# Kernel tuning notes

Hardware: AMD Instinct MI355X
Metric: run time of the kernel (lower is better)

Reference implementation:

```python
import jax, jax.numpy as jnp
import numpy as np

B, D, H, E, K = 8192, 1024, 256, 16, 4


def setup_inputs() -> dict:
    key = jax.random.key(0)
    ks = jax.random.split(key, 6)
    s_d = D ** -0.5
    s_h = H ** -0.5
    return {
        "x": jax.random.normal(ks[0], (B, D), dtype=jnp.float32),
        "route_w": jax.random.normal(ks[1], (E, D), dtype=jnp.float32) * s_d,
        "w1": jax.random.normal(ks[2], (E, H, D), dtype=jnp.float32) * s_d,
        "b1": jax.random.normal(ks[3], (E, H), dtype=jnp.float32) * s_d,
        "w2": jax.random.normal(ks[4], (E, D, H), dtype=jnp.float32) * s_h,
        "b2": jax.random.normal(ks[5], (E, D), dtype=jnp.float32) * s_h,
    }


def _moe_forward(x, route_w, w1, b1, w2, b2):
    # Router: logits (B, E) -> top-k softmax weights scattered back to (B, E).
    logits = x @ route_w.T
    top_vals, top_idx = jax.lax.top_k(logits, K)
    top_w = jax.nn.softmax(top_vals, axis=-1)
    rows = jnp.arange(x.shape[0])[:, None]
    weights = jnp.zeros_like(logits).at[rows, top_idx].set(top_w)  # (B, E)

    # Experts: out = sum_e w[:, e] * relu(relu(x W1e^T + b1e) W2e^T + b2e)
    # Non-selected experts have weight 0, so dense-then-weight matches the
    # original masked gather/scatter math exactly (dropout = 0).
    def step(out, params_e):
        W1, bb1, W2, bb2, we = params_e
        h = jax.nn.relu(x @ W1.T + bb1)       # (B, H)
        y = jax.nn.relu(h @ W2.T + bb2)       # (B, D)
        return out + y * we[:, None], None

    out0 = jnp.zeros_like(x)
    out, _ = jax.lax.scan(step, out0, (w1, b1, w2, b2, weights.T))
    return out


def reference(x, route_w, w1, b1, w2, b2):
    return _moe_forward(x, route_w, w1, b1, w2, b2)
```

## Files before the change

kernel.cpp:

```cpp
#include <hip/hip_runtime.h>
#include <stdint.h>

typedef unsigned short u16;
typedef __attribute__((ext_vector_type(8))) short bf16x8;
typedef __attribute__((ext_vector_type(4))) float f32x4;
typedef __attribute__((ext_vector_type(8))) u16 u16x8;
typedef __attribute__((ext_vector_type(4))) u16 u16x4;

#define NTOK 8192
#define DDIM 1024
#define HDIM 256
#define NEXP 16
#define MAXT 272
#define MAXSLOT (MAXT * 128)

__device__ __forceinline__ u16 f2bf(float f) {
  uint32_t u = __builtin_bit_cast(uint32_t, f);
  u += 0x7FFFu + ((u >> 16) & 1u);
  return (u16)(u >> 16);
}
__device__ __forceinline__ float bf2f(u16 h) {
  return __builtin_bit_cast(float, (uint32_t)h << 16);
}

__device__ __forceinline__ void gll16(const void* g, void* l) {
  __builtin_amdgcn_global_load_lds((const __attribute__((address_space(1))) void*)g,
                                   (__attribute__((address_space(3))) void*)l,
                                   16, 0, 0);
}

__global__ __launch_bounds__(256) void cvt_kernel(const float* __restrict__ in,
                                                  u16* __restrict__ out) {
  size_t i = ((size_t)blockIdx.x * 256 + threadIdx.x) * 8;
  const float4 a = *(const float4*)(in + i);
  const float4 b = *(const float4*)(in + i + 4);
  u16x8 o;
  o[0] = f2bf(a.x); o[1] = f2bf(a.y); o[2] = f2bf(a.z); o[3] = f2bf(a.w);
  o[4] = f2bf(b.x); o[5] = f2bf(b.y); o[6] = f2bf(b.z); o[7] = f2bf(b.w);
  *(u16x8*)(out + i) = o;
}

__global__ __launch_bounds__(256) void zero_out_kernel(float* __restrict__ p) {
  size_t i = ((size_t)blockIdx.x * 256 + threadIdx.x) * 4;
  *(float4*)(p + i) = (float4){0.f, 0.f, 0.f, 0.f};
}

__global__ __launch_bounds__(256) void router_kernel(const float* __restrict__ x,
                                                     const float* __restrict__ rw,
                                                     int* __restrict__ epack,
                                                     float* __restrict__ ew,
                                                     u16* __restrict__ xbf) {
  __shared__ __align__(16) uint8_t rwlds[65536];
  const int tid = threadIdx.x;

#pragma unroll
  for (int i = 0; i < 16; ++i) {
    int byte = (i * 256 + tid) * 16;
    int sw = byte ^ (((byte >> 8) & 7) << 4);
    *(float4*)(rwlds + sw) = *(const float4*)((const uint8_t*)rw + byte);
  }
  __syncthreads();

  const int lane = tid & 63, wid = tid >> 6;
  const int s = lane & 15;
  const int tok = blockIdx.x * 16 + wid * 4 + (lane >> 4);
  const float* xrow = x + (size_t)tok * DDIM;
  u16* xbrow = xbf + (size_t)tok * DDIM;

  double acc[NEXP];
#pragma unroll
  for (int e = 0; e < NEXP; ++e) acc[e] = 0.0;

#pragma unroll 4
  for (int g = 0; g < 16; ++g) {
    const int d = s * 64 + g * 4;
    float4 xv = *(const float4*)(xrow + d);
    u16x4 o;
    o[0] = f2bf(xv.x); o[1] = f2bf(xv.y); o[2] = f2bf(xv.z); o[3] = f2bf(xv.w);
    *(u16x4*)(xbrow + d) = o;
    const double x0 = xv.x, x1 = xv.y, x2 = xv.z, x3 = xv.w;
    const int roff = (s * 256 + g * 16) ^ ((s & 7) << 4);
#pragma unroll
    for (int e = 0; e < NEXP; ++e) {
      float4 rv = *(const float4*)(rwlds + e * 4096 + roff);
      acc[e] = fma(x0, (double)rv.x, acc[e]);
      acc[e] = fma(x1, (double)rv.y, acc[e]);
      acc[e] = fma(x2, (double)rv.z, acc[e]);
      acc[e] = fma(x3, (double)rv.w, acc[e]);
    }
  }

#define FOLD(H, M)                                                   \
  _Pragma("unroll") for (int i = 0; i < H; ++i) {                    \
    double send = (lane & M) ? acc[i] : acc[i + H];                  \
    double recv = __shfl_xor(send, M);                               \
    acc[i] = ((lane & M) ? acc[i + H] : acc[i]) + recv;              \
  }
  FOLD(8, 1)
  FOLD(4, 2)
  FOLD(2, 4)
  FOLD(1, 8)
#undef FOLD
  const int e_mine = ((lane & 1) << 3) | ((lane & 2) << 1) |
                     ((lane & 4) >> 1) | ((lane & 8) >> 3);

  double val = acc[0];
  double tv[4]; int tidx[4];
#pragma unroll
  for (int k = 0; k < 4; ++k) {
    double bv = val; int be = e_mine;
#pragma unroll
    for (int m = 1; m < 16; m <<= 1) {
      double ov = __shfl_xor(bv, m);
      int oe = __shfl_xor(be, m);
      if (ov > bv || (ov == bv && oe < be)) { bv = ov; be = oe; }
    }
    tv[k] = bv; tidx[k] = be;
    if (e_mine == be) val = -1.0e300;
  }

  if ((lane & 15) == 0) {
    float m0 = (float)tv[0];
    float w[4]; float sum = 0.f;
#pragma unroll
    for (int k = 0; k < 4; ++k) { w[k] = expf((float)tv[k] - m0); sum += w[k]; }
    epack[tok] = tidx[0] | (tidx[1] << 8) | (tidx[2] << 16) | (tidx[3] << 24);
#pragma unroll
    for (int k = 0; k < 4; ++k) ew[tok * 4 + k] = w[k] / sum;
  }
}

__global__ __launch_bounds__(1024) void compact_kernel(const int* __restrict__ epack,
                                                       const float* __restrict__ ew,
                                                       int* __restrict__ texp,
                                                       int* __restrict__ perm,
                                                       float* __restrict__ wsl,
                                                       int* __restrict__ islot) {
  __shared__ int wave_cnt[16][NEXP];
  __shared__ int counts_sm[NEXP];
  __shared__ int wtot[16], wave_off[16];
  const int e = blockIdx.x;
  const int tid = threadIdx.x, lane = tid & 63, w = tid >> 6;

  int ep[8]; unsigned m[8];
#pragma unroll
  for (int j = 0; j < 8; ++j) {
    ep[j] = epack[tid * 8 + j];
    m[j] = (1u << (ep[j] & 255)) | (1u << ((ep[j] >> 8) & 255)) |
           (1u << ((ep[j] >> 16) & 255)) | (1u << ((ep[j] >> 24) & 255));
  }
#pragma unroll
  for (int ee = 0; ee < NEXP; ++ee) {
    int c = 0;
#pragma unroll
    for (int j = 0; j < 8; ++j) c += (m[j] >> ee) & 1u;
#pragma unroll
    for (int off = 32; off > 0; off >>= 1) c += __shfl_xor(c, off);
    if (lane == 0) wave_cnt[w][ee] = c;
  }
  unsigned fm = 0;
#pragma unroll
  for (int j = 0; j < 8; ++j) fm |= ((m[j] >> e) & 1u) << j;
  int s = __popc(fm);
  int incl = s;
#pragma unroll
  for (int d = 1; d < 64; d <<= 1) {
    int t2 = __shfl_up(incl, d);
    if (lane >= d) incl += t2;
  }
  if (lane == 63) wtot[w] = incl;
  __syncthreads();
  if (tid < NEXP) {
    int c = 0;
    for (int w2 = 0; w2 < 16; ++w2) c += wave_cnt[w2][tid];
    counts_sm[tid] = c;
  }
  if (tid == 0) {
    int run = 0;
    for (int w2 = 0; w2 < 16; ++w2) { wave_off[w2] = run; run += wtot[w2]; }
  }
  __syncthreads();
  int base = 0;
  for (int ee = 0; ee < NEXP; ++ee)
    if (ee < e) base += ((counts_sm[ee] + 127) >> 7) << 7;
  int pos = base + wave_off[w] + (incl - s);
#pragma unroll
  for (int j = 0; j < 8; ++j) {
    if ((fm >> j) & 1u) {
      int tok = tid * 8 + j;
      int b0 = ep[j] & 255, b1 = (ep[j] >> 8) & 255, b2_ = (ep[j] >> 16) & 255;
      int k = (b0 == e) ? 0 : ((b1 == e) ? 1 : ((b2_ == e) ? 2 : 3));
      perm[pos] = tok;
      wsl[pos] = ew[tok * 4 + k];
      islot[tok * 4 + k] = pos;
      ++pos;
    }
  }
  int cnt = counts_sm[e];
  int pad = (((cnt + 127) >> 7) << 7) - cnt;
  if (tid < pad) { perm[base + cnt + tid] = 0; wsl[base + cnt + tid] = 0.f; }
  if (e == 0 && tid == 0) {
    int tc = 0;
    for (int ee = 0; ee < NEXP; ++ee) {
      int nt = (counts_sm[ee] + 127) >> 7;
      for (int i = 0; i < nt; ++i) texp[tc++] = ee;
    }
    for (; tc < MAXT; ++tc) texp[tc] = -1;
  }
}

__device__ __forceinline__ void stage_rows(const u16* __restrict__ base, int ld,
                                           int kbase, uint8_t* dst, int tid) {
#pragma unroll
  for (int i = 0; i < 4; ++i) {
    int u = i * 256 + tid;
    int row = u >> 3, g = u & 7;
    gll16(base + (size_t)row * ld + kbase + ((g ^ (row & 7)) << 3), dst + u * 16);
  }
}
__device__ __forceinline__ void stage_gather(const u16* __restrict__ xbf,
                                             const int tok[4], int kbase,
                                             uint8_t* dst, int tid) {
#pragma unroll
  for (int i = 0; i < 4; ++i) {
    int u = i * 256 + tid;
    int row = u >> 3, g = u & 7;
    gll16(xbf + (size_t)tok[i] * DDIM + kbase + ((g ^ (row & 7)) << 3), dst + u * 16);
  }
}

__device__ __forceinline__ void mma_tile(const uint8_t* Ab, const uint8_t* Bb,
                                         f32x4 acc[4][4], int wm, int wn,
                                         int lrow, int lk) {
#pragma unroll
  for (int s = 0; s < 2; ++s) {
    bf16x8 af[4], bfr[4];
#pragma unroll
    for (int f = 0; f < 4; ++f) {
      int ar = wm * 64 + f * 16 + lrow;
      af[f] = *(const bf16x8*)(Ab + ar * 128 + ((((s << 2) | lk) ^ (ar & 7)) << 4));
      int br = wn * 64 + f * 16 + lrow;
      bfr[f] = *(const bf16x8*)(Bb + br * 128 + ((((s << 2) | lk) ^ (br & 7)) << 4));
    }
#pragma unroll
    for (int i = 0; i < 4; ++i)
#pragma unroll
      for (int j = 0; j < 4; ++j)
        acc[i][j] = __builtin_amdgcn_mfma_f32_16x16x32_bf16(af[i], bfr[j], acc[i][j], 0, 0, 0);
  }
}

__global__ __launch_bounds__(256) void gemm1_kernel(const u16* __restrict__ xbf,
                                                    const u16* __restrict__ w1bf,
                                                    const float* __restrict__ b1,
                                                    const int* __restrict__ texp,
                                                    const int* __restrict__ perm,
                                                    u16* __restrict__ Hc, int t0) {
  __shared__ __align__(16) uint8_t smem[2][32768];
  const int t = t0 + blockIdx.x;
  const int e = (t < MAXT) ? texp[t] : -1;
  if (e < 0) return;
  const int n0 = blockIdx.y * 128;
  const int tid = threadIdx.x;
  const int lane = tid & 63, wid = tid >> 6;
  const int wm = wid >> 1, wn = wid & 1;
  const int lrow = lane & 15, lk = lane >> 4;

  int tok[4];
#pragma unroll
  for (int i = 0; i < 4; ++i) tok[i] = perm[t * 128 + ((i * 256 + tid) >> 3)];
  const u16* Bsrc = w1bf + ((size_t)e * HDIM + n0) * DDIM;

  f32x4 acc[4][4];
#pragma unroll
  for (int i = 0; i < 4; ++i)
#pragma unroll
    for (int j = 0; j < 4; ++j) acc[i][j] = (f32x4){0.f, 0.f, 0.f, 0.f};

  stage_gather(xbf, tok, 0, smem[0], tid);
  stage_rows(Bsrc, DDIM, 0, smem[0] + 16384, tid);
  __syncthreads();
  int cur = 0;
  for (int kt = 0; kt < 16; ++kt) {
    if (kt < 15) {
      stage_gather(xbf, tok, (kt + 1) * 64, smem[cur ^ 1], tid);
      stage_rows(Bsrc, DDIM, (kt + 1) * 64, smem[cur ^ 1] + 16384, tid);
    }
    mma_tile(smem[cur], smem[cur] + 16384, acc, wm, wn, lrow, lk);
    __syncthreads();
    cur ^= 1;
  }
#pragma unroll
  for (int j = 0; j < 4; ++j) {
    int n = n0 + wn * 64 + j * 16 + lrow;
    float bias = b1[e * HDIM + n];
#pragma unroll
    for (int i = 0; i < 4; ++i) {
      int rloc = blockIdx.x * 128 + wm * 64 + i * 16 + lk * 4;
#pragma unroll
      for (int r = 0; r < 4; ++r) {
        float h = fmaxf(acc[i][j][r] + bias, 0.f);
        Hc[((size_t)rloc + r) * HDIM + n] = f2bf(h);
      }
    }
  }
}

template <int MODE>
__global__ __launch_bounds__(256) void gemm2_kernel(const u16* __restrict__ Hc,
                                                    const u16* __restrict__ w2bf,
                                                    const float* __restrict__ b2,
                                                    const int* __restrict__ texp,
                                                    const int* __restrict__ perm,
                                                    const float* __restrict__ wsl,
                                                    float* __restrict__ out,
                                                    u16* __restrict__ ybuf,
                                                    int t0, int n0, int NC) {
  __shared__ __align__(16) uint8_t smem[2][32768];
  const int t = t0 + blockIdx.x;
  const int e = (t < MAXT) ? texp[t] : -1;
  if (e < 0) return;
  const int tid = threadIdx.x;
  const int lane = tid & 63, wid = tid >> 6;
  const int wm = wid >> 1, wn = wid & 1;
  const int lrow = lane & 15, lk = lane >> 4;

  const u16* Asrc = Hc + (size_t)blockIdx.x * 128 * HDIM;
  const u16* Bsrc = w2bf + ((size_t)e * DDIM + n0 + blockIdx.y * 128) * HDIM;

  f32x4 acc[4][4];
#pragma unroll
  for (int i = 0; i < 4; ++i)
#pragma unroll
    for (int j = 0; j < 4; ++j) acc[i][j] = (f32x4){0.f, 0.f, 0.f, 0.f};

  stage_rows(Asrc, HDIM, 0, smem[0], tid);
  stage_rows(Bsrc, HDIM, 0, smem[0] + 16384, tid);
  __syncthreads();
  int cur = 0;
  for (int kt = 0; kt < 4; ++kt) {
    if (kt < 3) {
      stage_rows(Asrc, HDIM, (kt + 1) * 64, smem[cur ^ 1], tid);
      stage_rows(Bsrc, HDIM, (kt + 1) * 64, smem[cur ^ 1] + 16384, tid);
    }
    mma_tile(smem[cur], smem[cur] + 16384, acc, wm, wn, lrow, lk);
    __syncthreads();
    cur ^= 1;
  }
  float bias[4];
#pragma unroll
  for (int j = 0; j < 4; ++j)
    bias[j] = b2[e * DDIM + n0 + blockIdx.y * 128 + wn * 64 + j * 16 + lrow];
#pragma unroll
  for (int i = 0; i < 4; ++i) {
#pragma unroll
    for (int r = 0; r < 4; ++r) {
      int slot = t * 128 + wm * 64 + i * 16 + lk * 4 + r;
      if (MODE == 0) {
        int tokn = perm[slot];
        float w = wsl[slot];
#pragma unroll
        for (int j = 0; j < 4; ++j) {
          int n = n0 + blockIdx.y * 128 + wn * 64 + j * 16 + lrow;
          float h = fmaxf(acc[i][j][r] + bias[j], 0.f);
          atomicAdd(&out[(size_t)tokn * DDIM + n], w * h);
        }
      } else {
#pragma unroll
        for (int j = 0; j < 4; ++j) {
          int nloc = blockIdx.y * 128 + wn * 64 + j * 16 + lrow;
          float h = fmaxf(acc[i][j][r] + bias[j], 0.f);
          ybuf[(size_t)slot * NC + nloc] = f2bf(h);
        }
      }
    }
  }
}

__global__ __launch_bounds__(256) void combine_kernel(const u16* __restrict__ ybuf,
                                                      const float* __restrict__ ew,
                                                      const int* __restrict__ islot,
                                                      float* __restrict__ out,
                                                      int n0, int NC, int cshift) {
  int gid = blockIdx.x * 256 + threadIdx.x;
  int t = gid >> cshift;
  int c = (gid & ((1 << cshift) - 1)) << 2;
  const int4 sl = *(const int4*)(islot + t * 4);
  const float4 w = *(const float4*)(ew + t * 4);
  float4 a = {0.f, 0.f, 0.f, 0.f};
#define ACC(SL, W)                                             \
  {                                                            \
    u16x4 y = *(const u16x4*)(ybuf + (size_t)(SL)*NC + c);     \
    a.x += (W)*bf2f(y[0]); a.y += (W)*bf2f(y[1]);              \
    a.z += (W)*bf2f(y[2]); a.w += (W)*bf2f(y[3]);              \
  }
  ACC(sl.x, w.x); ACC(sl.y, w.y); ACC(sl.z, w.z); ACC(sl.w, w.w);
#undef ACC
  *(float4*)(out + (size_t)t * DDIM + n0 + c) = a;
}

extern "C" void kernel_launch(void* const* d_in, const int* in_sizes, int n_in,
                              void* d_out, int out_size, void* d_ws, size_t ws_size,
                              hipStream_t stream) {
  const float* x = (const float*)d_in[0];
  const float* route_w = (const float*)d_in[1];
  const float* w1 = (const float*)d_in[2];
  const float* b1 = (const float*)d_in[3];
  const float* w2 = (const float*)d_in[4];
  const float* b2 = (const float*)d_in[5];
  float* out = (float*)d_out;

  uint8_t* ws = (uint8_t*)d_ws;
  const size_t OFF_EPACK = 0;
  const size_t OFF_EW    = 32768;
  const size_t OFF_ISLOT = 163840;
  const size_t OFF_TEXP  = 294912;
  const size_t OFF_PERM  = 296960;
  const size_t OFF_WSL   = 436224;
  const size_t OFF_X     = 1048576;
  const size_t OFF_W1    = OFF_X + (size_t)NTOK * DDIM * 2;
  const size_t OFF_W2    = OFF_W1 + (size_t)NEXP * HDIM * DDIM * 2;
  const size_t OFF_HC    = OFF_W2 + (size_t)NEXP * DDIM * HDIM * 2;
  const size_t OFF_Y     = OFF_HC + (size_t)MAXSLOT * HDIM * 2;

  int* epack  = (int*)(ws + OFF_EPACK);
  float* ew   = (float*)(ws + OFF_EW);
  int* islot  = (int*)(ws + OFF_ISLOT);
  int* texp   = (int*)(ws + OFF_TEXP);
  int* perm   = (int*)(ws + OFF_PERM);
  float* wsl  = (float*)(ws + OFF_WSL);
  u16* xbf    = (u16*)(ws + OFF_X);
  u16* w1bf   = (u16*)(ws + OFF_W1);
  u16* w2bf   = (u16*)(ws + OFF_W2);
  u16* Hc     = (u16*)(ws + OFF_HC);
  u16* ybuf   = (u16*)(ws + OFF_Y);

  cvt_kernel<<<dim3((NEXP * HDIM * DDIM) / 2048), 256, 0, stream>>>(w1, w1bf);
  cvt_kernel<<<dim3((NEXP * DDIM * HDIM) / 2048), 256, 0, stream>>>(w2, w2bf);
  router_kernel<<<dim3(NTOK / 16), 256, 0, stream>>>(x, route_w, epack, ew, xbf);
  compact_kernel<<<dim3(NEXP), 1024, 0, stream>>>(epack, ew, texp, perm, wsl, islot);

  int NC = 0;
  for (int cand = 1024; cand >= 128; cand >>= 1) {
    if (ws_size >= OFF_Y + (size_t)MAXSLOT * cand * 2) { NC = cand; break; }
  }

  if (NC > 0) {
    gemm1_kernel<<<dim3(MAXT, HDIM / 128), 256, 0, stream>>>(xbf, w1bf, b1, texp, perm, Hc, 0);
    int cshift = __builtin_ctz(NC >> 2);
    for (int n0 = 0; n0 < DDIM; n0 += NC) {
      gemm2_kernel<1><<<dim3(MAXT, NC / 128), 256, 0, stream>>>(
          Hc, w2bf, b2, texp, perm, wsl, out, ybuf, 0, n0, NC);
      combine_kernel<<<dim3((NTOK << cshift) / 256), 256, 0, stream>>>(
          ybuf, ew, islot, out, n0, NC, cshift);
    }
  } else {
    long room = (long)ws_size - (long)OFF_HC;
    int CT = (int)(room / 65536);
    if (CT > MAXT) CT = MAXT;
    if (CT < 16) CT = 16;
    zero_out_kernel<<<dim3((NTOK * DDIM) / 1024), 256, 0, stream>>>(out);
    for (int t0 = 0; t0 < MAXT; t0 += CT) {
      int ct = (MAXT - t0 < CT) ? (MAXT - t0) : CT;
      gemm1_kernel<<<dim3(ct, HDIM / 128), 256, 0, stream>>>(xbf, w1bf, b1, texp, perm, Hc, t0);
      gemm2_kernel<0><<<dim3(ct, DDIM / 128), 256, 0, stream>>>(
          Hc, w2bf, b2, texp, perm, wsl, out, ybuf, t0, 0, DDIM);
    }
  }
}
```

Before: 145.3 us.

## Keep H tile resident in LDS and sweep all output columns per block in GEMM2

Replaces the 2D-grid GEMM2 with a 512-thread kernel that loads the block's full 128x256 H tile into shared memory once, then streams W2 column chunks through a double buffer, writing each 128-column output chunk after its four k-steps. This removes the repeated reload of the H tile across column blocks and caps the ybuf chunk width at 512, so the combine pass runs in at least two rounds. In exchange it uses 96KB of LDS per block and launches only one block per token tile, which lowers parallelism and occupancy.

```diff
diff --git a/kernel.cpp b/kernel.cpp
--- a/kernel.cpp
+++ b/kernel.cpp
@@ -218,6 +218,15 @@
     gll16(base + (size_t)row * ld + kbase + ((g ^ (row & 7)) << 3), dst + u * 16);
   }
 }
+__device__ __forceinline__ void stage_rows512(const u16* __restrict__ base, int ld,
+                                              int kbase, uint8_t* dst, int tid) {
+#pragma unroll
+  for (int i = 0; i < 2; ++i) {
+    int u = i * 512 + tid;
+    int row = u >> 3, g = u & 7;
+    gll16(base + (size_t)row * ld + kbase + ((g ^ (row & 7)) << 3), dst + u * 16);
+  }
+}
 __device__ __forceinline__ void stage_gather(const u16* __restrict__ xbf,
                                              const int tok[4], int kbase,
                                              uint8_t* dst, int tid) {
@@ -244,6 +253,30 @@
     }
 #pragma unroll
     for (int i = 0; i < 4; ++i)
+#pragma unroll
+      for (int j = 0; j < 4; ++j)
+        acc[i][j] = __builtin_amdgcn_mfma_f32_16x16x32_bf16(af[i], bfr[j], acc[i][j], 0, 0, 0);
+  }
+}
+
+__device__ __forceinline__ void mma_step8(const uint8_t* Ab, const uint8_t* Bb,
+                                          f32x4 acc[2][4], int wm, int wn,
+                                          int lrow, int lk) {
+#pragma unroll
+  for (int s = 0; s < 2; ++s) {
+    bf16x8 af[2], bfr[4];
+#pragma unroll
+    for (int f = 0; f < 2; ++f) {
+      int ar = wm * 32 + f * 16 + lrow;
+      af[f] = *(const bf16x8*)(Ab + ar * 128 + ((((s << 2) | lk) ^ (ar & 7)) << 4));
+    }
+#pragma unroll
+    for (int f = 0; f < 4; ++f) {
+      int br = wn * 64 + f * 16 + lrow;
+      bfr[f] = *(const bf16x8*)(Bb + br * 128 + ((((s << 2) | lk) ^ (br & 7)) << 4));
+    }
+#pragma unroll
+    for (int i = 0; i < 2; ++i)
 #pragma unroll
       for (int j = 0; j < 4; ++j)
         acc[i][j] = __builtin_amdgcn_mfma_f32_16x16x32_bf16(af[i], bfr[j], acc[i][j], 0, 0, 0);
@@ -306,16 +339,75 @@
   }
 }
 
-template <int MODE>
-__global__ __launch_bounds__(256) void gemm2_kernel(const u16* __restrict__ Hc,
-                                                    const u16* __restrict__ w2bf,
-                                                    const float* __restrict__ b2,
-                                                    const int* __restrict__ texp,
-                                                    const int* __restrict__ perm,
-                                                    const float* __restrict__ wsl,
-                                                    float* __restrict__ out,
-                                                    u16* __restrict__ ybuf,
-                                                    int t0, int n0, int NC) {
+__global__ __launch_bounds__(512) void gemm2_wide_kernel(const u16* __restrict__ Hc,
+                                                         const u16* __restrict__ w2bf,
+                                                         const float* __restrict__ b2,
+                                                         const int* __restrict__ texp,
+                                                         u16* __restrict__ ybuf,
+                                                         int nbase, int ncols) {
+  __shared__ __align__(16) uint8_t smem[98304];
+  const int t = blockIdx.x;
+  const int e = texp[t];
+  if (e < 0) return;
+  const int tid = threadIdx.x;
+  const int lane = tid & 63, wid = tid >> 6;
+  const int wm = wid >> 1, wn = wid & 1;
+  const int lrow = lane & 15, lk = lane >> 4;
+
+  const u16* Asrc = Hc + (size_t)t * 128 * HDIM;
+#pragma unroll
+  for (int c = 0; c < 4; ++c)
+    stage_rows512(Asrc, HDIM, c * 64, smem + c * 16384, tid);
+
+  const u16* W2base = w2bf + ((size_t)e * DDIM + nbase) * HDIM;
+  const int S = ncols >> 5;
+  stage_rows512(W2base, HDIM, 0, smem + 65536, tid);
+  __syncthreads();
+
+  f32x4 acc[2][4];
+#pragma unroll
+  for (int i = 0; i < 2; ++i)
+#pragma unroll
+    for (int j = 0; j < 4; ++j) acc[i][j] = (f32x4){0.f, 0.f, 0.f, 0.f};
+
+  int cur = 0;
+  for (int s = 0; s < S; ++s) {
+    const int kt = s & 3, nc = s >> 2;
+    if (s + 1 < S) {
+      const int kt2 = (s + 1) & 3, nc2 = (s + 1) >> 2;
+      stage_rows512(W2base + (size_t)(nc2 * 128) * HDIM, HDIM, kt2 * 64,
+                    smem + 65536 + ((cur ^ 1) << 14), tid);
+    }
+    mma_step8(smem + (kt << 14), smem + 65536 + (cur << 14), acc, wm, wn, lrow, lk);
+    if (kt == 3) {
+#pragma unroll
+      for (int j = 0; j < 4; ++j) {
+        const int nl = nc * 128 + wn * 64 + j * 16 + lrow;
+        const float bias = b2[e * DDIM + nbase + nl];
+#pragma unroll
+        for (int i = 0; i < 2; ++i) {
+          const int slotb = t * 128 + wm * 32 + i * 16 + lk * 4;
+#pragma unroll
+          for (int r = 0; r < 4; ++r) {
+            float h = fmaxf(acc[i][j][r] + bias, 0.f);
+            ybuf[(size_t)(slotb + r) * ncols + nl] = f2bf(h);
+          }
+          acc[i][j] = (f32x4){0.f, 0.f, 0.f, 0.f};
+        }
+      }
+    }
+    __syncthreads();
+    cur ^= 1;
+  }
+}
+
+__global__ __launch_bounds__(256) void gemm2_fb_kernel(const u16* __restrict__ Hc,
+                                                       const u16* __restrict__ w2bf,
+                                                       const float* __restrict__ b2,
+                                                       const int* __restrict__ texp,
+                                                       const int* __restrict__ perm,
+                                                       const float* __restrict__ wsl,
+                                                       float* __restrict__ out, int t0) {
   __shared__ __align__(16) uint8_t smem[2][32768];
   const int t = t0 + blockIdx.x;
   const int e = (t < MAXT) ? texp[t] : -1;
@@ -326,7 +418,7 @@
   const int lrow = lane & 15, lk = lane >> 4;
 
   const u16* Asrc = Hc + (size_t)blockIdx.x * 128 * HDIM;
-  const u16* Bsrc = w2bf + ((size_t)e * DDIM + n0 + blockIdx.y * 128) * HDIM;
+  const u16* Bsrc = w2bf + ((size_t)e * DDIM + blockIdx.y * 128) * HDIM;
 
   f32x4 acc[4][4];
 #pragma unroll
@@ -350,28 +442,19 @@
   float bias[4];
 #pragma unroll
   for (int j = 0; j < 4; ++j)
-    bias[j] = b2[e * DDIM + n0 + blockIdx.y * 128 + wn * 64 + j * 16 + lrow];
+    bias[j] = b2[e * DDIM + blockIdx.y * 128 + wn * 64 + j * 16 + lrow];
 #pragma unroll
   for (int i = 0; i < 4; ++i) {
 #pragma unroll
     for (int r = 0; r < 4; ++r) {
       int slot = t * 128 + wm * 64 + i * 16 + lk * 4 + r;
-      if (MODE == 0) {
-        int tokn = perm[slot];
-        float w = wsl[slot];
-#pragma unroll
-        for (int j = 0; j < 4; ++j) {
-          int n = n0 + blockIdx.y * 128 + wn * 64 + j * 16 + lrow;
-          float h = fmaxf(acc[i][j][r] + bias[j], 0.f);
-          atomicAdd(&out[(size_t)tokn * DDIM + n], w * h);
-        }
-      } else {
-#pragma unroll
-        for (int j = 0; j < 4; ++j) {
-          int nloc = blockIdx.y * 128 + wn * 64 + j * 16 + lrow;
-          float h = fmaxf(acc[i][j][r] + bias[j], 0.f);
-          ybuf[(size_t)slot * NC + nloc] = f2bf(h);
-        }
+      int tokn = perm[slot];
+      float w = wsl[slot];
+#pragma unroll
+      for (int j = 0; j < 4; ++j) {
+        int n = blockIdx.y * 128 + wn * 64 + j * 16 + lrow;
+        float h = fmaxf(acc[i][j][r] + bias[j], 0.f);
+        atomicAdd(&out[(size_t)tokn * DDIM + n], w * h);
       }
     }
   }
@@ -440,19 +523,18 @@
   router_kernel<<<dim3(NTOK / 16), 256, 0, stream>>>(x, route_w, epack, ew, xbf);
   compact_kernel<<<dim3(NEXP), 1024, 0, stream>>>(epack, ew, texp, perm, wsl, islot);
 
-  int NC = 0;
-  for (int cand = 1024; cand >= 128; cand >>= 1) {
-    if (ws_size >= OFF_Y + (size_t)MAXSLOT * cand * 2) { NC = cand; break; }
-  }
-
-  if (NC > 0) {
+  int ybN = 0;
+  for (int cand = 512; cand >= 128; cand >>= 1) {
+    if (ws_size >= OFF_Y + (size_t)MAXSLOT * cand * 2) { ybN = cand; break; }
+  }
+
+  if (ybN > 0) {
     gemm1_kernel<<<dim3(MAXT, HDIM / 128), 256, 0, stream>>>(xbf, w1bf, b1, texp, perm, Hc, 0);
-    int cshift = __builtin_ctz(NC >> 2);
-    for (int n0 = 0; n0 < DDIM; n0 += NC) {
-      gemm2_kernel<1><<<dim3(MAXT, NC / 128), 256, 0, stream>>>(
-          Hc, w2bf, b2, texp, perm, wsl, out, ybuf, 0, n0, NC);
+    int cshift = __builtin_ctz(ybN >> 2);
+    for (int nb = 0; nb < DDIM; nb += ybN) {
+      gemm2_wide_kernel<<<dim3(MAXT), 512, 0, stream>>>(Hc, w2bf, b2, texp, ybuf, nb, ybN);
       combine_kernel<<<dim3((NTOK << cshift) / 256), 256, 0, stream>>>(
-          ybuf, ew, islot, out, n0, NC, cshift);
+          ybuf, ew, islot, out, nb, ybN, cshift);
     }
   } else {
     long room = (long)ws_size - (long)OFF_HC;
@@ -463,8 +545,8 @@
     for (int t0 = 0; t0 < MAXT; t0 += CT) {
       int ct = (MAXT - t0 < CT) ? (MAXT - t0) : CT;
       gemm1_kernel<<<dim3(ct, HDIM / 128), 256, 0, stream>>>(xbf, w1bf, b1, texp, perm, Hc, t0);
-      gemm2_kernel<0><<<dim3(ct, DDIM / 128), 256, 0, stream>>>(
-          Hc, w2bf, b2, texp, perm, wsl, out, ybuf, t0, 0, DDIM);
-    }
-  }
-}
+      gemm2_fb_kernel<<<dim3(ct, DDIM / 128), 256, 0, stream>>>(
+          Hc, w2bf, b2, texp, perm, wsl, out, t0);
+    }
+  }
+}
```

Result: slower. 170.1 us (+17.1%).

## Single-buffer GEMM LDS and swap grid axes so N-tiles of a token tile launch adjacently

Applied to the files above, without the earlier changes.

Replaces the double-buffered 64KB shared memory in the expert GEMM kernels with one 32KB buffer and a load-sync-compute-sync loop. This halves LDS per block so more blocks can be resident per CU. The grid axes are also swapped so that blocks sharing a token tile (same gathered A rows) are scheduled next to each other, which should improve L2 reuse of A. The gemm2 template is split into separate main and fallback kernels. The cost is that global loads no longer overlap the MFMA work within a block, so the kernel relies on inter-block occupancy to hide that latency.

```diff
diff --git a/kernel.cpp b/kernel.cpp
--- a/kernel.cpp
+++ b/kernel.cpp
@@ -256,11 +256,13 @@
                                                     const int* __restrict__ texp,
                                                     const int* __restrict__ perm,
                                                     u16* __restrict__ Hc, int t0) {
-  __shared__ __align__(16) uint8_t smem[2][32768];
-  const int t = t0 + blockIdx.x;
+  __shared__ __align__(16) uint8_t Ab[16384];
+  __shared__ __align__(16) uint8_t Bb[16384];
+  const int tl = blockIdx.y;
+  const int t = t0 + tl;
   const int e = (t < MAXT) ? texp[t] : -1;
   if (e < 0) return;
-  const int n0 = blockIdx.y * 128;
+  const int n0 = blockIdx.x * 128;
   const int tid = threadIdx.x;
   const int lane = tid & 63, wid = tid >> 6;
   const int wm = wid >> 1, wn = wid & 1;
@@ -277,18 +279,12 @@
 #pragma unroll
     for (int j = 0; j < 4; ++j) acc[i][j] = (f32x4){0.f, 0.f, 0.f, 0.f};
 
-  stage_gather(xbf, tok, 0, smem[0], tid);
-  stage_rows(Bsrc, DDIM, 0, smem[0] + 16384, tid);
-  __syncthreads();
-  int cur = 0;
   for (int kt = 0; kt < 16; ++kt) {
-    if (kt < 15) {
-      stage_gather(xbf, tok, (kt + 1) * 64, smem[cur ^ 1], tid);
-      stage_rows(Bsrc, DDIM, (kt + 1) * 64, smem[cur ^ 1] + 16384, tid);
-    }
-    mma_tile(smem[cur], smem[cur] + 16384, acc, wm, wn, lrow, lk);
+    stage_gather(xbf, tok, kt * 64, Ab, tid);
+    stage_rows(Bsrc, DDIM, kt * 64, Bb, tid);
     __syncthreads();
-    cur ^= 1;
+    mma_tile(Ab, Bb, acc, wm, wn, lrow, lk);
+    __syncthreads();
   }
 #pragma unroll
   for (int j = 0; j < 4; ++j) {
@@ -296,7 +292,7 @@
     float bias = b1[e * HDIM + n];
 #pragma unroll
     for (int i = 0; i < 4; ++i) {
-      int rloc = blockIdx.x * 128 + wm * 64 + i * 16 + lk * 4;
+      int rloc = tl * 128 + wm * 64 + i * 16 + lk * 4;
 #pragma unroll
       for (int r = 0; r < 4; ++r) {
         float h = fmaxf(acc[i][j][r] + bias, 0.f);
@@ -306,18 +302,69 @@
   }
 }
 
-template <int MODE>
-__global__ __launch_bounds__(256) void gemm2_kernel(const u16* __restrict__ Hc,
-                                                    const u16* __restrict__ w2bf,
-                                                    const float* __restrict__ b2,
-                                                    const int* __restrict__ texp,
-                                                    const int* __restrict__ perm,
-                                                    const float* __restrict__ wsl,
-                                                    float* __restrict__ out,
-                                                    u16* __restrict__ ybuf,
-                                                    int t0, int n0, int NC) {
-  __shared__ __align__(16) uint8_t smem[2][32768];
-  const int t = t0 + blockIdx.x;
+__global__ __launch_bounds__(256) void gemm2_main_kernel(const u16* __restrict__ Hc,
+                                                         const u16* __restrict__ w2bf,
+                                                         const float* __restrict__ b2,
+                                                         const int* __restrict__ texp,
+                                                         u16* __restrict__ ybuf,
+                                                         int nbase, int NC) {
+  __shared__ __align__(16) uint8_t Ab[16384];
+  __shared__ __align__(16) uint8_t Bb[16384];
+  const int t = blockIdx.y;
+  const int e = texp[t];
+  if (e < 0) return;
+  const int nl0 = blockIdx.x * 128;
+  const int tid = threadIdx.x;
+  const int lane = tid & 63, wid = tid >> 6;
+  const int wm = wid >> 1, wn = wid & 1;
+  const int lrow = lane & 15, lk = lane >> 4;
+
+  const u16* Asrc = Hc + (size_t)t * 128 * HDIM;
+  const u16* Bsrc = w2bf + ((size_t)e * DDIM + nbase + nl0) * HDIM;
+
+  f32x4 acc[4][4];
+#pragma unroll
+  for (int i = 0; i < 4; ++i)
+#pragma unroll
+    for (int j = 0; j < 4; ++j) acc[i][j] = (f32x4){0.f, 0.f, 0.f, 0.f};
+
+  for (int kt = 0; kt < 4; ++kt) {
+    stage_rows(Asrc, HDIM, kt * 64, Ab, tid);
+    stage_rows(Bsrc, HDIM, kt * 64, Bb, tid);
+    __syncthreads();
+    mma_tile(Ab, Bb, acc, wm, wn, lrow, lk);
+    __syncthreads();
+  }
+  float bias[4];
+#pragma unroll
+  for (int j = 0; j < 4; ++j)
+    bias[j] = b2[e * DDIM + nbase + nl0 + wn * 64 + j * 16 + lrow];
+#pragma unroll
+  for (int i = 0; i < 4; ++i) {
+#pragma unroll
+    for (int r = 0; r < 4; ++r) {
+      int slot = t * 128 + wm * 64 + i * 16 + lk * 4 + r;
+#pragma unroll
+      for (int j = 0; j < 4; ++j) {
+        int nloc = nl0 + wn * 64 + j * 16 + lrow;
+        float h = fmaxf(acc[i][j][r] + bias[j], 0.f);
+        ybuf[(size_t)slot * NC + nloc] = f2bf(h);
+      }
+    }
+  }
+}
+
+__global__ __launch_bounds__(256) void gemm2_fb_kernel(const u16* __restrict__ Hc,
+                                                       const u16* __restrict__ w2bf,
+                                                       const float* __restrict__ b2,
+                                                       const int* __restrict__ texp,
+                                                       const int* __restrict__ perm,
+                                                       const float* __restrict__ wsl,
+                                                       float* __restrict__ out, int t0) {
+  __shared__ __align__(16) uint8_t Ab[16384];
+  __shared__ __align__(16) uint8_t Bb[16384];
+  const int tl = blockIdx.y;
+  const int t = t0 + tl;
   const int e = (t < MAXT) ? texp[t] : -1;
   if (e < 0) return;
   const int tid = threadIdx.x;
@@ -325,8 +372,8 @@
   const int wm = wid >> 1, wn = wid & 1;
   const int lrow = lane & 15, lk = lane >> 4;
 
-  const u16* Asrc = Hc + (size_t)blockIdx.x * 128 * HDIM;
-  const u16* Bsrc = w2bf + ((size_t)e * DDIM + n0 + blockIdx.y * 128) * HDIM;
+  const u16* Asrc = Hc + (size_t)tl * 128 * HDIM;
+  const u16* Bsrc = w2bf + ((size_t)e * DDIM + blockIdx.x * 128) * HDIM;
 
   f32x4 acc[4][4];
 #pragma unroll
@@ -334,44 +381,29 @@
 #pragma unroll
     for (int j = 0; j < 4; ++j) acc[i][j] = (f32x4){0.f, 0.f, 0.f, 0.f};
 
-  stage_rows(Asrc, HDIM, 0, smem[0], tid);
-  stage_rows(Bsrc, HDIM, 0, smem[0] + 16384, tid);
-  __syncthreads();
-  int cur = 0;
   for (int kt = 0; kt < 4; ++kt) {
-    if (kt < 3) {
-      stage_rows(Asrc, HDIM, (kt + 1) * 64, smem[cur ^ 1], tid);
-      stage_rows(Bsrc, HDIM, (kt + 1) * 64, smem[cur ^ 1] + 16384, tid);
-    }
-    mma_tile(smem[cur], smem[cur] + 16384, acc, wm, wn, lrow, lk);
+    stage_rows(Asrc, HDIM, kt * 64, Ab, tid);
+    stage_rows(Bsrc, HDIM, kt * 64, Bb, tid);
     __syncthreads();
-    cur ^= 1;
+    mma_tile(Ab, Bb, acc, wm, wn, lrow, lk);
+    __syncthreads();
   }
   float bias[4];
 #pragma unroll
   for (int j = 0; j < 4; ++j)
-    bias[j] = b2[e * DDIM + n0 + blockIdx.y * 128 + wn * 64 + j * 16 + lrow];
+    bias[j] = b2[e * DDIM + blockIdx.x * 128 + wn * 64 + j * 16 + lrow];
 #pragma unroll
   for (int i = 0; i < 4; ++i) {
 #pragma unroll
     for (int r = 0; r < 4; ++r) {
       int slot = t * 128 + wm * 64 + i * 16 + lk * 4 + r;
-      if (MODE == 0) {
-        int tokn = perm[slot];
-        float w = wsl[slot];
-#pragma unroll
-        for (int j = 0; j < 4; ++j) {
-          int n = n0 + blockIdx.y * 128 + wn * 64 + j * 16 + lrow;
-          float h = fmaxf(acc[i][j][r] + bias[j], 0.f);
-          atomicAdd(&out[(size_t)tokn * DDIM + n], w * h);
-        }
-      } else {
-#pragma unroll
-        for (int j = 0; j < 4; ++j) {
-          int nloc = blockIdx.y * 128 + wn * 64 + j * 16 + lrow;
-          float h = fmaxf(acc[i][j][r] + bias[j], 0.f);
-          ybuf[(size_t)slot * NC + nloc] = f2bf(h);
-        }
+      int tokn = perm[slot];
+      float w = wsl[slot];
+#pragma unroll
+      for (int j = 0; j < 4; ++j) {
+        int n = blockIdx.x * 128 + wn * 64 + j * 16 + lrow;
+        float h = fmaxf(acc[i][j][r] + bias[j], 0.f);
+        atomicAdd(&out[(size_t)tokn * DDIM + n], w * h);
       }
     }
   }
@@ -440,19 +472,19 @@
   router_kernel<<<dim3(NTOK / 16), 256, 0, stream>>>(x, route_w, epack, ew, xbf);
   compact_kernel<<<dim3(NEXP), 1024, 0, stream>>>(epack, ew, texp, perm, wsl, islot);
 
-  int NC = 0;
+  int ybN = 0;
   for (int cand = 1024; cand >= 128; cand >>= 1) {
-    if (ws_size >= OFF_Y + (size_t)MAXSLOT * cand * 2) { NC = cand; break; }
-  }
-
-  if (NC > 0) {
-    gemm1_kernel<<<dim3(MAXT, HDIM / 128), 256, 0, stream>>>(xbf, w1bf, b1, texp, perm, Hc, 0);
-    int cshift = __builtin_ctz(NC >> 2);
-    for (int n0 = 0; n0 < DDIM; n0 += NC) {
-      gemm2_kernel<1><<<dim3(MAXT, NC / 128), 256, 0, stream>>>(
-          Hc, w2bf, b2, texp, perm, wsl, out, ybuf, 0, n0, NC);
+    if (ws_size >= OFF_Y + (size_t)MAXSLOT * cand * 2) { ybN = cand; break; }
+  }
+
+  if (ybN > 0) {
+    gemm1_kernel<<<dim3(HDIM / 128, MAXT), 256, 0, stream>>>(xbf, w1bf, b1, texp, perm, Hc, 0);
+    int cshift = __builtin_ctz(ybN >> 2);
+    for (int nb = 0; nb < DDIM; nb += ybN) {
+      gemm2_main_kernel<<<dim3(ybN / 128, MAXT), 256, 0, stream>>>(
+          Hc, w2bf, b2, texp, ybuf, nb, ybN);
       combine_kernel<<<dim3((NTOK << cshift) / 256), 256, 0, stream>>>(
-          ybuf, ew, islot, out, n0, NC, cshift);
+          ybuf, ew, islot, out, nb, ybN, cshift);
     }
   } else {
     long room = (long)ws_size - (long)OFF_HC;
@@ -462,9 +494,9 @@
     zero_out_kernel<<<dim3((NTOK * DDIM) / 1024), 256, 0, stream>>>(out);
     for (int t0 = 0; t0 < MAXT; t0 += CT) {
       int ct = (MAXT - t0 < CT) ? (MAXT - t0) : CT;
-      gemm1_kernel<<<dim3(ct, HDIM / 128), 256, 0, stream>>>(xbf, w1bf, b1, texp, perm, Hc, t0);
-      gemm2_kernel<0><<<dim3(ct, DDIM / 128), 256, 0, stream>>>(
-          Hc, w2bf, b2, texp, perm, wsl, out, ybuf, t0, 0, DDIM);
-    }
-  }
-}
+      gemm1_kernel<<<dim3(HDIM / 128, ct), 256, 0, stream>>>(xbf, w1bf, b1, texp, perm, Hc, t0);
+      gemm2_fb_kernel<<<dim3(DDIM / 128, ct), 256, 0, stream>>>(
+          Hc, w2bf, b2, texp, perm, wsl, out, t0);
+    }
+  }
+}
```

Result: slower. 150.6 us (+3.6%).
